# Kernel optimization log

Measured on AMD Instinct MI355X. Metric: run time of the kernel, lower is better.

## Reference

```python
import jax, jax.numpy as jnp
import numpy as np

NUM_USERS = 100000
NUM_POIS = 50000
DIM = 128
NUM_EDGES = 3_200_000


def setup_inputs() -> dict:
    key = jax.random.key(0)
    ks = jax.random.split(key, 8)
    return {
        "user_idx": jax.random.randint(ks[0], (1,), 0, NUM_USERS, dtype=jnp.int64 if jax.config.jax_enable_x64 else jnp.int32).astype(jnp.int32),
        "poi_embeddings": jax.random.normal(ks[1], (NUM_POIS, DIM), dtype=jnp.float32),
        "edge_src": jax.random.randint(ks[2], (NUM_EDGES,), 0, NUM_USERS, dtype=jnp.int32),
        "edge_dst": jax.random.randint(ks[3], (NUM_EDGES,), 0, NUM_POIS, dtype=jnp.int32),
        "edge_freq": jax.random.randint(ks[4], (NUM_EDGES,), 1, 50, dtype=jnp.int32),
        "user_emb": jax.random.normal(ks[5], (NUM_USERS, DIM), dtype=jnp.float32),
        "fc_w": jax.random.normal(ks[6], (DIM, 2 * DIM), dtype=jnp.float32) * (1.0 / np.sqrt(2 * DIM)),
        "fc_b": jax.random.normal(ks[7], (DIM,), dtype=jnp.float32) * 0.01,
    }


def reference(user_idx, poi_embeddings, edge_src, edge_dst, edge_freq, user_emb, fc_w, fc_b):
    # user embedding lookup: [1, d]
    u = user_emb[user_idx]
    # mask edges belonging to this user, weights = visit frequencies
    mask = edge_src == user_idx[0]
    w = jnp.where(mask, edge_freq.astype(jnp.float32), 0.0)  # [E]
    # scatter masked frequencies onto POI ids, then one [P] x [P,d] contraction
    # == sum over matched edges of freq * poi_embeddings[dst]
    acc = jnp.zeros((poi_embeddings.shape[0],), poi_embeddings.dtype).at[edge_dst].add(w)
    num = acc @ poi_embeddings  # [d]
    denom = w.sum()
    safe = jnp.where(denom > 0, denom, 1.0)
    neigh = jnp.where(denom > 0, num / safe, 0.0)[None, :]  # [1, d]; zeros if no edges
    combined = jnp.concatenate([u, neigh], axis=1)  # [1, 2d]
    return combined @ fc_w.T + fc_b
```

## Files before the change

### kernel.cpp

```cpp
#include <hip/hip_runtime.h>

#define CAP 8192
#define DIM 128

__global__ void filter_edges_kernel(const int* __restrict__ user_idx,
                                    const int* __restrict__ edge_src,
                                    const int* __restrict__ edge_dst,
                                    const int* __restrict__ edge_freq,
                                    int E,
                                    int* __restrict__ count,
                                    int* __restrict__ mdst,
                                    int* __restrict__ mfreq) {
    const int uid = user_idx[0];
    const int gtid = blockIdx.x * blockDim.x + threadIdx.x;
    const int stride = gridDim.x * blockDim.x;
    const int E4 = E >> 2;
    const int4* __restrict__ src4 = (const int4*)edge_src;

    for (int i4 = gtid; i4 < E4; i4 += stride) {
        int4 s = src4[i4];
        if (s.x == uid || s.y == uid || s.z == uid || s.w == uid) {
            const int base = i4 * 4;
            int vals[4] = {s.x, s.y, s.z, s.w};
#pragma unroll
            for (int j = 0; j < 4; ++j) {
                if (vals[j] == uid) {
                    int p = atomicAdd(count, 1);
                    if (p < CAP) {
                        mdst[p]  = edge_dst[base + j];
                        mfreq[p] = edge_freq[base + j];
                    }
                }
            }
        }
    }
    for (int i = E4 * 4 + gtid; i < E; i += stride) {
        if (edge_src[i] == uid) {
            int p = atomicAdd(count, 1);
            if (p < CAP) {
                mdst[p]  = edge_dst[i];
                mfreq[p] = edge_freq[i];
            }
        }
    }
}

__global__ void __launch_bounds__(DIM)
finish_kernel(const int* __restrict__ user_idx,
              const float* __restrict__ poi,
              const float* __restrict__ user_emb,
              const float* __restrict__ fc_w,
              const float* __restrict__ fc_b,
              const int* __restrict__ count,
              const int* __restrict__ mdst,
              const int* __restrict__ mfreq,
              float* __restrict__ out) {
    __shared__ float comb[2 * DIM];
    const int d = threadIdx.x;

    int cnt = *count;
    if (cnt > CAP) cnt = CAP;

    float num = 0.0f;
    float den = 0.0f;
    for (int m = 0; m < cnt; ++m) {
        const float f = (float)mfreq[m];
        num += f * poi[(size_t)mdst[m] * DIM + d];
        den += f;
    }
    const float neigh = (den > 0.0f) ? (num / den) : 0.0f;

    const int uid = user_idx[0];
    comb[d]       = user_emb[(size_t)uid * DIM + d];
    comb[DIM + d] = neigh;
    __syncthreads();

    const float4* __restrict__ w4 = (const float4*)(fc_w + (size_t)d * (2 * DIM));
    float acc = fc_b[d];
#pragma unroll 8
    for (int k = 0; k < (2 * DIM) / 4; ++k) {
        const float4 w = w4[k];
        acc += w.x * comb[4 * k + 0] + w.y * comb[4 * k + 1] +
               w.z * comb[4 * k + 2] + w.w * comb[4 * k + 3];
    }
    out[d] = acc;
}

extern "C" void kernel_launch(void* const* d_in, const int* in_sizes, int n_in,
                              void* d_out, int out_size, void* d_ws, size_t ws_size,
                              hipStream_t stream) {
    const int*   user_idx  = (const int*)d_in[0];
    const float* poi       = (const float*)d_in[1];
    const int*   edge_src  = (const int*)d_in[2];
    const int*   edge_dst  = (const int*)d_in[3];
    const int*   edge_freq = (const int*)d_in[4];
    const float* user_emb  = (const float*)d_in[5];
    const float* fc_w      = (const float*)d_in[6];
    const float* fc_b      = (const float*)d_in[7];
    float* out = (float*)d_out;

    const int E = in_sizes[2];

    char* ws = (char*)d_ws;
    int* count = (int*)ws;
    int* mdst  = (int*)(ws + 64);
    int* mfreq = (int*)(ws + 64 + 4 * CAP);

    hipMemsetAsync(count, 0, sizeof(int), stream);

    const int threads = 256;
    const int E4 = E >> 2;
    int blocks = (E4 + threads - 1) / threads;
    if (blocks < 1) blocks = 1;
    if (blocks > 65535) blocks = 65535;

    filter_edges_kernel<<<blocks, threads, 0, stream>>>(
        user_idx, edge_src, edge_dst, edge_freq, E, count, mdst, mfreq);

    finish_kernel<<<1, DIM, 0, stream>>>(
        user_idx, poi, user_emb, fc_w, fc_b, count, mdst, mfreq, out);
}
```

Measured before the change: 147.3 us.

## Fuse neighbor aggregation into edge scan with wave-cooperative float atomics

Instead of compacting matched edges into a buffer and aggregating them in a single-block finish kernel, the scan kernel now has each wavefront ballot over matched edges and cooperatively gather the POI row, atomically adding freq-weighted values into a global accumulator. This moves the serial aggregation off the single 128-thread block and into the parallel scan. It adds global float atomics, which are contended on 129 addresses and make the summation order nondeterministic. It also removes the CAP limit on matched edges.

```diff
diff --git a/kernel.cpp b/kernel.cpp
--- a/kernel.cpp
+++ b/kernel.cpp
@@ -1,74 +1,73 @@
 #include <hip/hip_runtime.h>
 
-#define CAP 8192
 #define DIM 128
 
-__global__ void filter_edges_kernel(const int* __restrict__ user_idx,
-                                    const int* __restrict__ edge_src,
-                                    const int* __restrict__ edge_dst,
-                                    const int* __restrict__ edge_freq,
-                                    int E,
-                                    int* __restrict__ count,
-                                    int* __restrict__ mdst,
-                                    int* __restrict__ mfreq) {
+
+__global__ void scan_accum_kernel(const int* __restrict__ user_idx,
+                                  const int* __restrict__ edge_src,
+                                  const int* __restrict__ edge_dst,
+                                  const int* __restrict__ edge_freq,
+                                  int E,
+                                  const float* __restrict__ poi,
+                                  float* __restrict__ num,
+                                  float* __restrict__ den) {
     const int uid = user_idx[0];
+    const int lane = threadIdx.x & 63;
     const int gtid = blockIdx.x * blockDim.x + threadIdx.x;
     const int stride = gridDim.x * blockDim.x;
     const int E4 = E >> 2;
     const int4* __restrict__ src4 = (const int4*)edge_src;
 
     for (int i4 = gtid; i4 < E4; i4 += stride) {
-        int4 s = src4[i4];
-        if (s.x == uid || s.y == uid || s.z == uid || s.w == uid) {
+        const int4 s = src4[i4];
+        const bool any = (s.x == uid) | (s.y == uid) | (s.z == uid) | (s.w == uid);
+        if (__any(any)) {
             const int base = i4 * 4;
-            int vals[4] = {s.x, s.y, s.z, s.w};
+            const int sv[4] = {s.x, s.y, s.z, s.w};
 #pragma unroll
             for (int j = 0; j < 4; ++j) {
-                if (vals[j] == uid) {
-                    int p = atomicAdd(count, 1);
-                    if (p < CAP) {
-                        mdst[p]  = edge_dst[base + j];
-                        mfreq[p] = edge_freq[base + j];
-                    }
+                const bool m = (sv[j] == uid);
+                int dst = 0, f = 0;
+                if (m) { dst = edge_dst[base + j]; f = edge_freq[base + j]; }
+                unsigned long long b = __ballot(m);
+                while (b) {
+                    const int sl = (int)__ffsll(b) - 1;
+                    b &= b - 1;
+                    const int   ddst = __shfl(dst, sl);
+                    const float fv   = (float)__shfl(f, sl);
+                    const float* row = poi + (size_t)ddst * DIM;
+                    const float v0 = row[lane];
+                    const float v1 = row[lane + 64];
+                    atomicAdd(&num[lane],      fv * v0);
+                    atomicAdd(&num[lane + 64], fv * v1);
+                    if (lane == 0) atomicAdd(den, fv);
                 }
             }
         }
     }
     for (int i = E4 * 4 + gtid; i < E; i += stride) {
         if (edge_src[i] == uid) {
-            int p = atomicAdd(count, 1);
-            if (p < CAP) {
-                mdst[p]  = edge_dst[i];
-                mfreq[p] = edge_freq[i];
-            }
+            const float fv = (float)edge_freq[i];
+            const float* row = poi + (size_t)edge_dst[i] * DIM;
+            for (int k = 0; k < DIM; ++k) atomicAdd(&num[k], fv * row[k]);
+            atomicAdd(den, fv);
         }
     }
 }
 
 __global__ void __launch_bounds__(DIM)
 finish_kernel(const int* __restrict__ user_idx,
-              const float* __restrict__ poi,
               const float* __restrict__ user_emb,
               const float* __restrict__ fc_w,
               const float* __restrict__ fc_b,
-              const int* __restrict__ count,
-              const int* __restrict__ mdst,
-              const int* __restrict__ mfreq,
+              const float* __restrict__ num,
+              const float* __restrict__ den,
               float* __restrict__ out) {
     __shared__ float comb[2 * DIM];
     const int d = threadIdx.x;
 
-    int cnt = *count;
-    if (cnt > CAP) cnt = CAP;
-
-    float num = 0.0f;
-    float den = 0.0f;
-    for (int m = 0; m < cnt; ++m) {
-        const float f = (float)mfreq[m];
-        num += f * poi[(size_t)mdst[m] * DIM + d];
-        den += f;
-    }
-    const float neigh = (den > 0.0f) ? (num / den) : 0.0f;
+    const float dv = *den;
+    const float neigh = (dv > 0.0f) ? (num[d] / dv) : 0.0f;
 
     const int uid = user_idx[0];
     comb[d]       = user_emb[(size_t)uid * DIM + d];
@@ -102,11 +101,10 @@
     const int E = in_sizes[2];
 
     char* ws = (char*)d_ws;
-    int* count = (int*)ws;
-    int* mdst  = (int*)(ws + 64);
-    int* mfreq = (int*)(ws + 64 + 4 * CAP);
+    float* num = (float*)ws;
+    float* den = (float*)(ws + 512);
 
-    hipMemsetAsync(count, 0, sizeof(int), stream);
+    hipMemsetAsync(ws, 0, 640, stream);
 
     const int threads = 256;
     const int E4 = E >> 2;
@@ -114,9 +112,9 @@
     if (blocks < 1) blocks = 1;
     if (blocks > 65535) blocks = 65535;
 
-    filter_edges_kernel<<<blocks, threads, 0, stream>>>(
-        user_idx, edge_src, edge_dst, edge_freq, E, count, mdst, mfreq);
+    scan_accum_kernel<<<blocks, threads, 0, stream>>>(
+        user_idx, edge_src, edge_dst, edge_freq, E, poi, num, den);
 
     finish_kernel<<<1, DIM, 0, stream>>>(
-        user_idx, poi, user_emb, fc_w, fc_b, count, mdst, mfreq, out);
+        user_idx, user_emb, fc_w, fc_b, num, den, out);
 }
```

Result: faster. 133.8 us, median of 2 (-9.2%).
